# Optimization experiments

Measured on AMD Instinct MI355X. Metric: run time of the kernel, lower is better.

Reference implementation:

```python
import jax, jax.numpy as jnp
import numpy as np

B, T, NQ, NT = 64, 256, 32, 32
NR = NQ - 1          # queries 1..31 are matched (query 0 = ego)
BIG = jnp.float32(1e6)   # cost for invalid (padded) target columns
W_CLASS, W_POS, W_VEL = 1.0, 5.0, 2.0


def setup_inputs() -> dict:
    key = jax.random.key(0)
    k1, k2, k3, k4, k5 = jax.random.split(key, 5)
    position = jax.random.normal(k1, (B, T, NQ, 3), jnp.float32)
    velocity = jax.random.normal(k2, (B, T, NQ, 3), jnp.float32)
    class_logits = jax.random.normal(k3, (B, T, NQ, 5), jnp.float32)
    targets = jax.random.normal(k4, (B, T, NT, 18), jnp.float32)
    # raw: 0 = invalid (all-zero onehot), 1 = ego (onehot idx 0), 2..4 -> onehot idx 1..3
    raw = jax.random.randint(k5, (B, T, NT), 0, 5)
    onehot = jnp.where(raw[..., None] > 0,
                       jax.nn.one_hot(jnp.maximum(raw - 1, 0), 4, dtype=jnp.float32),
                       0.0)
    targets = targets.at[..., 14:18].set(onehot)
    return {"position": position, "velocity": velocity,
            "class_logits": class_logits, "targets": targets}


def _cost_and_valid(position, velocity, class_logits, targets):
    # drop ego query 0
    pred_pos = position[:, :, 1:, :]          # [B,T,NR,3]
    pred_vel = velocity[:, :, 1:, :]
    probs = jax.nn.softmax(class_logits[:, :, 1:, :], axis=-1)   # [B,T,NR,5]
    tgt_pos = targets[..., 0:3]               # [B,T,NT,3]
    tgt_vel = targets[..., 3:6]
    oh = targets[..., 14:18]
    s = oh.sum(-1)
    idx4 = jnp.argmax(oh, -1)
    cls5 = jnp.where(s == 0, 0, idx4 + 1)     # [B,T,NT], 5-way class index
    valid = (s > 0) & (cls5 != 1)             # drop empty + ego targets
    # cost_class[b,t,q,j] = -probs[b,t,q,cls5[b,t,j]]
    cls_ix = jnp.broadcast_to(cls5[:, :, None, :, None], (B, T, NR, NT, 1))
    cost_cls = -jnp.take_along_axis(probs[:, :, :, None, :], cls_ix, axis=-1)[..., 0]
    cost_pos = jnp.abs(pred_pos[:, :, :, None, :] - tgt_pos[:, :, None, :, :]).sum(-1)
    cost_vel = jnp.abs(pred_vel[:, :, :, None, :] - tgt_vel[:, :, None, :, :]).sum(-1)
    C = W_CLASS * cost_cls + W_POS * cost_pos + W_VEL * cost_vel   # [B,T,NR,NT]
    return C, valid


def _lap(cost):
    # Jonker-Volgenant / Hungarian shortest augmenting path (e-maxx formulation),
    # rectangular n <= m. cost: [n, m]. Returns row2col [n] int32.
    n, m = cost.shape
    INF = jnp.float32(1e18)
    a = jnp.zeros((n + 1, m + 1), jnp.float32).at[1:, 1:].set(cost)  # 1-indexed
    cols = jnp.arange(m + 1, dtype=jnp.int32)

    def outer(i, uvp):
        u, v, p = uvp                      # potentials + p[j] = row matched to col j
        p = p.at[0].set(i)
        st = (u, v, p, jnp.full(m + 1, INF), jnp.zeros(m + 1, bool),
              jnp.zeros(m + 1, jnp.int32), jnp.int32(0))

        def cond(st):
            return st[2][st[6]] != 0

        def body(st):
            u, v, p, minv, used, way, j0 = st
            used = used.at[j0].set(True)
            i0 = p[j0]
            cur = a[i0] - u[i0] - v                       # reduced costs, [m+1]
            upd = (~used) & (cols > 0) & (cur < minv)
            minv = jnp.where(upd, cur, minv)
            way = jnp.where(upd, j0, way)
            cand = jnp.where(used | (cols == 0), INF, minv)
            j1 = jnp.argmin(cand).astype(jnp.int32)
            delta = cand[j1]
            u = u.at[p].add(jnp.where(used, delta, 0.0))
            v = v - jnp.where(used, delta, 0.0)
            minv = jnp.where(used, minv, minv - delta)
            return (u, v, p, minv, used, way, j1)

        u, v, p, _, _, way, j0 = jax.lax.while_loop(cond, body, st)

        def aug_body(s):
            p, j0 = s
            j1 = way[j0]
            return p.at[j0].set(p[j1]), j1

        p, _ = jax.lax.while_loop(lambda s: s[1] != 0, aug_body, (p, j0))
        return (u, v, p)

    u0 = jnp.zeros(n + 1, jnp.float32)
    v0 = jnp.zeros(m + 1, jnp.float32)
    p0 = jnp.zeros(m + 1, jnp.int32)
    _, _, p = jax.lax.fori_loop(1, n + 1, lambda i, c: outer(jnp.int32(i), c), (u0, v0, p0))
    # invert: p[j] = row -> row2col[row] = j (skip virtual col 0; free cols map to dummy row 0)
    row2col = jnp.zeros(n + 1, jnp.int32).at[p[1:]].set(cols[1:])
    return row2col[1:] - 1                                # 0-based col per row


@jax.jit
def _forward(position, velocity, class_logits, targets):
    C, valid = _cost_and_valid(position, velocity, class_logits, targets)
    # invalid target columns padded with a constant BIG cost; since it is constant
    # per column the optimal sub-assignment on valid columns equals scipy's
    # linear_sum_assignment on the valid-only rectangular matrix.
    Cm = jnp.where(valid[:, :, None, :], C, BIG)
    row2col = jax.vmap(_lap)(Cm.reshape(-1, NR, NT)).reshape(B, T, NR)  # [B,T,NR]
    assigned_valid = jnp.take_along_axis(valid, row2col, axis=-1)       # [B,T,NR]
    pred_idx = jnp.where(assigned_valid, jnp.arange(1, NQ, dtype=jnp.int32), -1)
    tgt_idx = jnp.where(assigned_valid, row2col, -1)
    return C, pred_idx, tgt_idx


def reference(position, velocity, class_logits, targets):
    # Returns (cost tensor [B,T,NR,NT], pred_idx [B,T,NR], tgt_idx [B,T,NR]).
    # (pred_idx[b,t,k], tgt_idx[b,t,k]) with pred_idx != -1 are the matched pairs,
    # equivalent to the original's per-frame (pred_indices, target_indices) lists.
    return _forward(position, velocity, class_logits, targets)
```

## Files before the change

### kernel.cpp

```cpp
#include <hip/hip_runtime.h>
#include <cmath>

#define NPROB 16384
#define PROBS_PER_BLOCK 4

template<int CTRL>
__device__ __forceinline__ float fmin_dpp(float x) {
  int s = __builtin_amdgcn_update_dpp(0, __float_as_int(x), CTRL, 0xF, 0xF, true);
  return fminf(x, __int_as_float(s));
}

typedef int v2i_t __attribute__((ext_vector_type(2)));
__device__ __forceinline__ float halfmin32(float x) {
  x = fmin_dpp<0xB1>(x);
  x = fmin_dpp<0x4E>(x);
  x = fmin_dpp<0x141>(x);
  x = fmin_dpp<0x140>(x);
#if __has_builtin(__builtin_amdgcn_permlane16_swap)
  v2i_t r = __builtin_amdgcn_permlane16_swap(__float_as_int(x), __float_as_int(x),
                                             false, false);
  return fminf(__int_as_float(r.x), __int_as_float(r.y));
#else
  int s = __builtin_amdgcn_ds_swizzle(__float_as_int(x), 0x401F);
  return fminf(x, __int_as_float(s));
#endif
}

__device__ __forceinline__ int bperm_i(int addr, int v) {
  return __builtin_amdgcn_ds_bpermute(addr, v);
}
__device__ __forceinline__ float bperm_f(int addr, float v) {
  return __int_as_float(__builtin_amdgcn_ds_bpermute(addr, __float_as_int(v)));
}

__device__ __forceinline__ int half_ctz(unsigned long long bal, bool hiHalf) {
  const int jlo = __builtin_ctz((unsigned)bal | 0x80000000u);
  const int jhi = __builtin_ctz((unsigned)(bal >> 32) | 0x80000000u);
  return hiHalf ? jhi : jlo;
}

__global__ __launch_bounds__(128, 5) void matcher_kernel(
    const float* __restrict__ position,
    const float* __restrict__ velocity,
    const float* __restrict__ logits,
    const float* __restrict__ targets,
    float* __restrict__ out)
{
#pragma clang fp contract(off)
  __shared__ float sCm[PROBS_PER_BLOCK][992];

  const int tid  = threadIdx.x;
  const int lane = tid & 63;
  const int rel  = lane & 31;
  const int hs   = lane & 32;
  const int hs4  = hs * 4;
  const bool hiHalf = (hs != 0);
  const int relp1 = rel + 1;
  const int lp   = tid >> 5;
  const int bt   = blockIdx.x * PROBS_PER_BLOCK + lp;

  const float* pos = position + (size_t)bt * 96;
  const float* vel = velocity + (size_t)bt * 96;
  const float* lg  = logits   + (size_t)bt * 160;
  const float* tg  = targets  + (size_t)bt * 576;

  const float* trow = tg + rel * 18;
  const float tp0 = trow[0],  tp1 = trow[1],  tp2 = trow[2];
  const float tv0 = trow[3],  tv1 = trow[4],  tv2 = trow[5];
  const float o0  = trow[14], o1  = trow[15], o2  = trow[16], o3 = trow[17];
  const float ssum = ((o0 + o1) + o2) + o3;
  const float mxo  = fmaxf(fmaxf(fmaxf(o0, o1), o2), o3);
  const int idx4 = (o0 == mxo) ? 0 : ((o1 == mxo) ? 1 : ((o2 == mxo) ? 2 : 3));
  const int cls5 = (ssum == 0.0f) ? 0 : (idx4 + 1);
  const int validc = (ssum > 0.0f && cls5 != 1) ? 1 : 0;

  float m_l = 0.0f, s_l = 1.0f;
  if (rel < 31) {
    const float* lr = lg + (rel + 1) * 5;
    const float l0 = lr[0], l1 = lr[1], l2 = lr[2], l3 = lr[3], l4 = lr[4];
    m_l = fmaxf(fmaxf(fmaxf(fmaxf(l0, l1), l2), l3), l4);
    const float e0 = expf(l0 - m_l), e1 = expf(l1 - m_l), e2 = expf(l2 - m_l),
                e3 = expf(l3 - m_l), e4 = expf(l4 - m_l);
    s_l = (((e0 + e1) + e2) + e3) + e4;
  }

  float* outC  = out + (size_t)bt * 992;
  float* cmrow = &sCm[lp][0];
  for (int r = 0; r < 31; ++r) {
    const float m_r = __shfl(m_l, hs + r, 64);
    const float s_r = __shfl(s_l, hs + r, 64);
    const float lgl = lg[(r + 1) * 5 + cls5];
    const float psel = expf(lgl - m_r) / s_r;
    const float pr0 = pos[(r + 1) * 3 + 0], pr1 = pos[(r + 1) * 3 + 1], pr2 = pos[(r + 1) * 3 + 2];
    const float vr0 = vel[(r + 1) * 3 + 0], vr1 = vel[(r + 1) * 3 + 1], vr2 = vel[(r + 1) * 3 + 2];
    const float cp = (fabsf(pr0 - tp0) + fabsf(pr1 - tp1)) + fabsf(pr2 - tp2);
    const float cv = (fabsf(vr0 - tv0) + fabsf(vr1 - tv1)) + fabsf(vr2 - tv2);
    const float Cv = (-psel + 5.0f * cp) + 2.0f * cv;
    outC[r * 32 + rel]  = Cv;
    cmrow[r * 32 + rel] = validc ? Cv : 1000000.0f;
  }

  const float INF = 1e18f;
  float u = 0.0f;
  float v = 0.0f;
  int   p = 0;

  const float* cmb = cmrow + rel - 32;

  for (int i = 1; i <= 31; ++i) {
    const float uq = bperm_f(hs4 + 4 * p - 4, u);
    const float u_i = __shfl(u, hs + (i - 1), 64);

    bool  used = false;
    float rowf = (rel == i - 1) ? 1.0f : 0.0f;
    int   way  = -1;

    float mv = (cmb[i * 32] - u_i) - v;
    const float mval = halfmin32(mv);
    int j0 = half_ctz(__ballot(mv == mval), hiHalf);
    u = fmaf(rowf, mval, u);
    mv -= mval;
    int   pj = bperm_i(hs4 + 4 * j0, p);
    float u0 = bperm_f(hs4 + 4 * j0, uq);

    while (pj != 0) {
      const bool pop = (rel == j0);
      used = used || pop;
      mv = pop ? INF : mv;
      rowf = (relp1 == pj) ? 1.0f : rowf;
      const float a2 = cmb[pj * 32];
      const float c2 = used ? INF : ((a2 - u0) - v);
      if (c2 < mv) { mv = c2; way = j0; }
      const float mv2 = halfmin32(mv);
      j0 = half_ctz(__ballot(mv == mv2), hiHalf);
      const float dv = used ? mv2 : 0.0f;
      u = fmaf(rowf, mv2, u);
      v -= dv;
      mv -= mv2;
      pj = bperm_i(hs4 + 4 * j0, p);
      u0 = bperm_f(hs4 + 4 * j0, uq);
    }

    while (true) {
      const int w1 = __shfl(way, hs + j0, 64);
      const int pv = __shfl(p, hs + ((w1 < 0) ? 0 : w1), 64);
      const int pja = (w1 < 0) ? i : pv;
      if (rel == j0) p = pja;
      if (w1 < 0) break;
      j0 = w1;
    }
  }

  const int dsta = (p > 0) ? (hs4 + 4 * (p - 1)) : 0x7ffc;
  const int col  = __builtin_amdgcn_ds_permute(dsta, rel);
  const int colc = col & 31;
  const int av   = __shfl(validc, hs + colc, 64);
  if (rel < 31) {
    const size_t base1 = (size_t)NPROB * 992;
    const size_t base2 = base1 + (size_t)NPROB * 31;
    out[base1 + (size_t)bt * 31 + rel] = av ? (float)(rel + 1) : -1.0f;
    out[base2 + (size_t)bt * 31 + rel] = av ? (float)col : -1.0f;
  }
}

extern "C" void kernel_launch(void* const* d_in, const int* in_sizes, int n_in,
                              void* d_out, int out_size, void* d_ws, size_t ws_size,
                              hipStream_t stream) {
  const float* position = (const float*)d_in[0];
  const float* velocity = (const float*)d_in[1];
  const float* logits   = (const float*)d_in[2];
  const float* targets  = (const float*)d_in[3];
  float* out = (float*)d_out;
  matcher_kernel<<<NPROB / PROBS_PER_BLOCK, 128, 0, stream>>>(
      position, velocity, logits, targets, out);
}
```

Before: 381.2 us.

## Flatten Hungarian loops into per-half-wave state machine to reduce divergence stalls

Replaces the nested row, augment and path-update loops with a single flat loop driven by per-lane state (i, j0, pj, done). Each wave holds two independent assignment problems, one per half. With the flat loop each half advances one step per iteration, so one half no longer idles until the other finishes its augmenting search or path update. The cost is a wave-wide vote every iteration and execution of both branch bodies whenever the halves are in different phases.

```diff
diff --git a/kernel.cpp b/kernel.cpp
--- a/kernel.cpp
+++ b/kernel.cpp
@@ -107,23 +107,14 @@
 
   const float* cmb = cmrow + rel - 32;
 
-  for (int i = 1; i <= 31; ++i) {
-    const float uq = bperm_f(hs4 + 4 * p - 4, u);
-    const float u_i = __shfl(u, hs + (i - 1), 64);
+  float uq = 0.0f, u_i = 0.0f, rowf = 0.0f, mv = 0.0f, u0 = 0.0f;
+  int   way = -1, j0 = -1, pj = 0, i = 0;
+  bool  used = false, done = false;
 
-    bool  used = false;
-    float rowf = (rel == i - 1) ? 1.0f : 0.0f;
-    int   way  = -1;
+  for (;;) {
+    if (__all(done)) break;
 
-    float mv = (cmb[i * 32] - u_i) - v;
-    const float mval = halfmin32(mv);
-    int j0 = half_ctz(__ballot(mv == mval), hiHalf);
-    u = fmaf(rowf, mval, u);
-    mv -= mval;
-    int   pj = bperm_i(hs4 + 4 * j0, p);
-    float u0 = bperm_f(hs4 + 4 * j0, uq);
-
-    while (pj != 0) {
+    if (pj != 0) {
       const bool pop = (rel == j0);
       used = used || pop;
       mv = pop ? INF : mv;
@@ -139,15 +130,31 @@
       mv -= mv2;
       pj = bperm_i(hs4 + 4 * j0, p);
       u0 = bperm_f(hs4 + 4 * j0, uq);
-    }
-
-    while (true) {
-      const int w1 = __shfl(way, hs + j0, 64);
-      const int pv = __shfl(p, hs + ((w1 < 0) ? 0 : w1), 64);
-      const int pja = (w1 < 0) ? i : pv;
-      if (rel == j0) p = pja;
-      if (w1 < 0) break;
-      j0 = w1;
+    } else if (!done) {
+      if (j0 >= 0) {
+        const int w1 = __shfl(way, hs + j0, 64);
+        const int pv = __shfl(p, hs + ((w1 < 0) ? 0 : w1), 64);
+        if (rel == j0) p = (w1 < 0) ? i : pv;
+        j0 = (w1 < 0) ? -1 : w1;
+      } else {
+        i += 1;
+        if (i > 31) {
+          done = true;
+        } else {
+          uq  = bperm_f(hs4 + 4 * p - 4, u);
+          u_i = __shfl(u, hs + (i - 1), 64);
+          used = false;
+          rowf = (rel == i - 1) ? 1.0f : 0.0f;
+          way  = -1;
+          mv = (cmb[i * 32] - u_i) - v;
+          const float mval = halfmin32(mv);
+          j0 = half_ctz(__ballot(mv == mval), hiHalf);
+          u = fmaf(rowf, mval, u);
+          mv -= mval;
+          pj = bperm_i(hs4 + 4 * j0, p);
+          u0 = bperm_f(hs4 + 4 * j0, uq);
+        }
+      }
     }
   }
 
```

Measured after the change: 503.3 us. 32.0% more time.
